# Kernel optimization log

Hardware: AMD Instinct MI355X
Metric: run time of the kernel (lower is better)

Reference implementation:

```python
import jax, jax.numpy as jnp
import numpy as np

# dims: B=batch, N1=in_channels (primary caps), P=pcap_n_dims, N2=n_caps, D=n_dims
B, N1, P, N2, D = 64, 1152, 8, 128, 16
ROUTINGS = 2


def squash(s, axis=-1):
    # squash_factor * unit_vector, with eps-stabilized norm (matches torch.finfo eps)
    sq_norm = jnp.sum(s * s, axis=axis, keepdims=True)
    norm = jnp.sqrt(sq_norm + jnp.finfo(s.dtype).eps)
    return (sq_norm / (1.0 + sq_norm)) * (s / norm)


def setup_inputs() -> dict:
    key = jax.random.key(0)
    k1, k2 = jax.random.split(key)
    x = jax.random.normal(k1, (B, N1, P), dtype=jnp.float32)
    # learned transform W: nn.Parameter(torch.randn(1, N1, N2, D, P)); leading 1 dropped
    W = jax.random.normal(k2, (N1, N2, D, P), dtype=jnp.float32)
    return {"x": x, "W": W}


def reference(x, W):
    b, n1 = x.shape[0], x.shape[1]
    n2 = W.shape[1]
    # caps2_predicted[b,i,n,d] = sum_p W[i,n,d,p] * x[b,i,p]  (the tiled batched matmul)
    pred = jnp.einsum('indp,bip->bind', W, x)  # [B, N1, N2, D]
    raw = jnp.zeros((b, n1, n2), dtype=pred.dtype)  # routing logits
    v = None
    for i in range(ROUTINGS):
        c = jax.nn.softmax(raw, axis=2)                  # softmax over output capsules
        s = jnp.einsum('bin,bind->bnd', c, pred)         # weighted sum over input caps
        v = squash(s, axis=-1)                           # [B, N2, D]
        if i < ROUTINGS - 1:
            # agreement: <prediction, output> over the D dimension
            raw = raw + jnp.einsum('bind,bnd->bin', pred, v)
    return v  # [B, n_caps, n_dims]
```

## Files before the change

### kernel.cpp

```cpp
#include <hip/hip_runtime.h>
#include <math.h>

#define B_   64
#define P_   8
#define N1_  1152
#define N2_  128
#define D_   16

#define NSPLIT 16
#define CHUNK  (N1_ / NSPLIT)
#define NIB    (CHUNK / 4)

typedef __attribute__((ext_vector_type(8)))  short bf16x8;
typedef __attribute__((ext_vector_type(4)))  float f32x4;
typedef __attribute__((ext_vector_type(16))) float f32x16;

__device__ inline void split_frag(float4 a0, float4 a1, bf16x8& hi, bf16x8& lo)
{
    float w[8] = {a0.x, a0.y, a0.z, a0.w, a1.x, a1.y, a1.z, a1.w};
#pragma unroll
    for (int j = 0; j < 8; ++j) {
        unsigned ub = __float_as_uint(w[j]);
        hi[j] = (short)(ub >> 16);
        float hif = __uint_as_float(ub & 0xffff0000u);
        float r = w[j] - hif;
        lo[j] = (short)(__float_as_uint(r) >> 16);
    }
}

__device__ inline void split_arr(const float* w, bf16x8& hi, bf16x8& lo)
{
#pragma unroll
    for (int j = 0; j < 8; ++j) {
        unsigned ub = __float_as_uint(w[j]);
        hi[j] = (short)(ub >> 16);
        float hif = __uint_as_float(ub & 0xffff0000u);
        float r = w[j] - hif;
        lo[j] = (short)(__float_as_uint(r) >> 16);
    }
}

__device__ inline void split4_pack(float4 s, uint2& hp, uint2& lp)
{
    float w[4] = {s.x, s.y, s.z, s.w};
    unsigned hs[4], ls[4];
#pragma unroll
    for (int j = 0; j < 4; ++j) {
        unsigned ub = __float_as_uint(w[j]);
        hs[j] = ub >> 16;
        float hif = __uint_as_float(ub & 0xffff0000u);
        float r = w[j] - hif;
        ls[j] = __float_as_uint(r) >> 16;
    }
    hp.x = hs[0] | (hs[1] << 16); hp.y = hs[2] | (hs[3] << 16);
    lp.x = ls[0] | (ls[1] << 16); lp.y = ls[2] | (ls[3] << 16);
}

__device__ inline unsigned short bf16_rne(float x, float& deq)
{
    unsigned ub = __float_as_uint(x);
    unsigned r  = ub + 0x7fffu + ((ub >> 16) & 1u);
    unsigned short us = (unsigned short)(r >> 16);
    deq = __uint_as_float(((unsigned)us) << 16);
    return us;
}

__global__ __launch_bounds__(256) void k1_s0_mfma(const float* __restrict__ x,
                                                  const float* __restrict__ W,
                                                  float* __restrict__ s0p)
{
    const int tid   = threadIdx.x;
    const int lane  = tid & 63;
    const int wv    = tid >> 6;
    const int col   = lane & 15;
    const int quad  = lane >> 4;
    const int n     = blockIdx.x * 4 + wv;
    const int isp   = blockIdx.y;
    const int ibase = isp * CHUNK;

    f32x4 acc[4];
#pragma unroll
    for (int bt = 0; bt < 4; ++bt) acc[bt] = (f32x4){0.f, 0.f, 0.f, 0.f};

    for (int ib = 0; ib < NIB; ++ib) {
        const int iq = ibase + ib * 4 + quad;
        const float* wp = W + ((size_t)iq * N2_ + n) * (D_ * P_) + col * P_;
        float4 wa = *(const float4*)wp;
        float4 wb = *(const float4*)(wp + 4);
        bf16x8 ahi, alo;
        split_frag(wa, wb, ahi, alo);
#pragma unroll
        for (int bt = 0; bt < 4; ++bt) {
            const int b = bt * 16 + col;
            const float* xp = x + ((size_t)b * N1_ + iq) * P_;
            float4 xa = *(const float4*)xp;
            float4 xb = *(const float4*)(xp + 4);
            bf16x8 bhi, blo;
            split_frag(xa, xb, bhi, blo);
            acc[bt] = __builtin_amdgcn_mfma_f32_16x16x32_bf16(ahi, bhi, acc[bt], 0, 0, 0);
            acc[bt] = __builtin_amdgcn_mfma_f32_16x16x32_bf16(ahi, blo, acc[bt], 0, 0, 0);
            acc[bt] = __builtin_amdgcn_mfma_f32_16x16x32_bf16(alo, bhi, acc[bt], 0, 0, 0);
        }
    }
#pragma unroll
    for (int bt = 0; bt < 4; ++bt) {
        const int b = bt * 16 + col;
        float4 v = make_float4(acc[bt][0], acc[bt][1], acc[bt][2], acc[bt][3]);
        *(float4*)(s0p + (size_t)isp * (B_ * N2_ * D_) + (size_t)b * (N2_ * D_)
                   + n * D_ + quad * 4) = v;
    }
}

__global__ __launch_bounds__(256) void k2_squash(const float* __restrict__ spart,
                                                 float* __restrict__ vout,
                                                 unsigned short* __restrict__ v0h,
                                                 unsigned short* __restrict__ v0l,
                                                 float scale, int nsplit)
{
    int idx = blockIdx.x * 256 + threadIdx.x;
    float4 s = make_float4(0.f, 0.f, 0.f, 0.f);
    for (int sp = 0; sp < nsplit; ++sp) {
        float4 t = *(const float4*)(spart + (size_t)sp * (B_ * N2_ * D_) + (size_t)idx * 4);
        s.x += t.x; s.y += t.y; s.z += t.z; s.w += t.w;
    }
    s.x *= scale; s.y *= scale; s.z *= scale; s.w *= scale;
    float sq = s.x * s.x + s.y * s.y + s.z * s.z + s.w * s.w;
    sq += __shfl_xor(sq, 1);
    sq += __shfl_xor(sq, 2);
    float norm = sqrtf(sq + 1.1920929e-7f);
    float f = (sq / (1.f + sq)) / norm;
    float4 o = make_float4(s.x * f, s.y * f, s.z * f, s.w * f);
    *(float4*)(vout + (size_t)idx * 4) = o;
    if (v0h) {
        uint2 hp, lp;
        split4_pack(o, hp, lp);
        *(uint2*)(v0h + (size_t)idx * 4) = hp;
        *(uint2*)(v0l + (size_t)idx * 4) = lp;
    }
}

__global__ __launch_bounds__(1024) void k3a2_mfma32(const float* __restrict__ x,
                                                    const float* __restrict__ W,
                                                    const unsigned short* __restrict__ v0h,
                                                    const unsigned short* __restrict__ v0l,
                                                    unsigned short* __restrict__ e_t,
                                                    float* __restrict__ denom)
{
    const int tid  = threadIdx.x;
    const int lane = tid & 63;
    const int wv   = tid >> 6;
    const int m    = lane & 31;
    const int kh   = lane >> 5;
    const int isub = m >> 3;
    const int p    = m & 7;
    const int i0   = blockIdx.x * 4;
    const int nbase = wv * 8;

    float4 xq0[4], xq1[4];
#pragma unroll
    for (int is = 0; is < 4; ++is) {
        xq0[is] = *(const float4*)(x + ((size_t)m * N1_ + i0 + is) * P_ + kh * 4);
        xq1[is] = *(const float4*)(x + ((size_t)(32 + m) * N1_ + i0 + is) * P_ + kh * 4);
    }

    float dacc[4] = {0.f, 0.f, 0.f, 0.f};

#pragma unroll 1
    for (int nt = 0; nt < 8; ++nt) {
        const int n = nbase + nt;

        bf16x8 vhi[2], vlo[2];
#pragma unroll
        for (int bt = 0; bt < 2; ++bt) {
            const size_t vo = (size_t)(bt * 32 + m) * (N2_ * D_) + n * D_ + kh * 8;
            vhi[bt] = *(const bf16x8*)(v0h + vo);
            vlo[bt] = *(const bf16x8*)(v0l + vo);
        }

        const float* wp = W + ((size_t)(i0 + isub) * N2_ + n) * (D_ * P_) + kh * 64 + p;
        float a[8];
#pragma unroll
        for (int j = 0; j < 8; ++j) a[j] = wp[8 * j];
        bf16x8 ahi, alo;
        split_arr(a, ahi, alo);

        f32x16 acc0, acc1;
#pragma unroll
        for (int r = 0; r < 16; ++r) { acc0[r] = 0.f; acc1[r] = 0.f; }
        acc0 = __builtin_amdgcn_mfma_f32_32x32x16_bf16(ahi, vhi[0], acc0, 0, 0, 0);
        acc0 = __builtin_amdgcn_mfma_f32_32x32x16_bf16(ahi, vlo[0], acc0, 0, 0, 0);
        acc0 = __builtin_amdgcn_mfma_f32_32x32x16_bf16(alo, vhi[0], acc0, 0, 0, 0);
        acc1 = __builtin_amdgcn_mfma_f32_32x32x16_bf16(ahi, vhi[1], acc1, 0, 0, 0);
        acc1 = __builtin_amdgcn_mfma_f32_32x32x16_bf16(ahi, vlo[1], acc1, 0, 0, 0);
        acc1 = __builtin_amdgcn_mfma_f32_32x32x16_bf16(alo, vhi[1], acc1, 0, 0, 0);

#pragma unroll
        for (int is = 0; is < 4; ++is) {
            float r0 = acc0[4 * is] * xq0[is].x + acc0[4 * is + 1] * xq0[is].y
                     + acc0[4 * is + 2] * xq0[is].z + acc0[4 * is + 3] * xq0[is].w;
            float r1 = acc1[4 * is] * xq1[is].x + acc1[4 * is + 1] * xq1[is].y
                     + acc1[4 * is + 2] * xq1[is].z + acc1[4 * is + 3] * xq1[is].w;
            r0 += __shfl_xor(r0, 32);
            r1 += __shfl_xor(r1, 32);
            float e = __expf(kh ? r1 : r0);
            float er;
            unsigned short eb = bf16_rne(e, er);
            e_t[(size_t)(i0 + is) * (N2_ * 64) + n * 64 + kh * 32 + m] = eb;
            dacc[is] += er;
        }
    }

    __shared__ float dred[16][4][64];
#pragma unroll
    for (int is = 0; is < 4; ++is) dred[wv][is][kh * 32 + m] = dacc[is];
    __syncthreads();
    if (tid < 256) {
        const int is = tid >> 6;
        const int b  = tid & 63;
        float s = 0.f;
#pragma unroll
        for (int w = 0; w < 16; ++w) s += dred[w][is][b];
        denom[(size_t)(i0 + is) * 64 + b] = s;
    }
}

__global__ __launch_bounds__(256) void k3c_s1_mfma(const float* __restrict__ x,
                                                   const float* __restrict__ W,
                                                   const unsigned short* __restrict__ e_t,
                                                   const float* __restrict__ denom,
                                                   float* __restrict__ s1p)
{
    const int tid   = threadIdx.x;
    const int lane  = tid & 63;
    const int wv    = tid >> 6;
    const int col   = lane & 15;
    const int quad  = lane >> 4;
    const int n     = blockIdx.x * 4 + wv;
    const int isp   = blockIdx.y;
    const int ibase = isp * CHUNK;

    f32x4 acc[4];
#pragma unroll
    for (int bt = 0; bt < 4; ++bt) acc[bt] = (f32x4){0.f, 0.f, 0.f, 0.f};

    for (int ib = 0; ib < NIB; ++ib) {
        const int iq = ibase + ib * 4 + quad;
        const float* wp = W + ((size_t)iq * N2_ + n) * (D_ * P_) + col * P_;
        float4 wa = *(const float4*)wp;
        float4 wb = *(const float4*)(wp + 4);
        bf16x8 ahi, alo;
        split_frag(wa, wb, ahi, alo);
#pragma unroll
        for (int bt = 0; bt < 4; ++bt) {
            const int b = bt * 16 + col;
            const float* xp = x + ((size_t)b * N1_ + iq) * P_;
            float4 xa = *(const float4*)xp;
            float4 xb = *(const float4*)(xp + 4);
            float e  = __uint_as_float((unsigned)e_t[((size_t)iq * N2_ + n) * 64 + b] << 16);
            float dv = denom[(size_t)iq * 64 + b];
            float c  = e * __builtin_amdgcn_rcpf(dv);
            float4 ya = make_float4(xa.x * c, xa.y * c, xa.z * c, xa.w * c);
            float4 yb = make_float4(xb.x * c, xb.y * c, xb.z * c, xb.w * c);
            bf16x8 bhi, blo;
            split_frag(ya, yb, bhi, blo);
            acc[bt] = __builtin_amdgcn_mfma_f32_16x16x32_bf16(ahi, bhi, acc[bt], 0, 0, 0);
            acc[bt] = __builtin_amdgcn_mfma_f32_16x16x32_bf16(ahi, blo, acc[bt], 0, 0, 0);
            acc[bt] = __builtin_amdgcn_mfma_f32_16x16x32_bf16(alo, bhi, acc[bt], 0, 0, 0);
        }
    }
#pragma unroll
    for (int bt = 0; bt < 4; ++bt) {
        const int b = bt * 16 + col;
        float4 v = make_float4(acc[bt][0], acc[bt][1], acc[bt][2], acc[bt][3]);
        *(float4*)(s1p + (size_t)isp * (B_ * N2_ * D_) + (size_t)b * (N2_ * D_)
                   + n * D_ + quad * 4) = v;
    }
}

extern "C" void kernel_launch(void* const* d_in, const int* in_sizes, int n_in,
                              void* d_out, int out_size, void* d_ws, size_t ws_size,
                              hipStream_t stream)
{
    const float* x = (const float*)d_in[0];
    const float* W = (const float*)d_in[1];
    float* out = (float*)d_out;

    float* s_part = (float*)d_ws;
    float* v0     = s_part + (size_t)NSPLIT * B_ * N2_ * D_;
    float* denom  = v0 + B_ * N2_ * D_;
    unsigned short* v0h = (unsigned short*)(denom + (size_t)N1_ * 64);
    unsigned short* v0l = v0h + (size_t)B_ * N2_ * D_;
    unsigned short* e_t = v0l + (size_t)B_ * N2_ * D_;

    k1_s0_mfma  <<<dim3(32, NSPLIT),  256, 0, stream>>>(x, W, s_part);
    k2_squash   <<<128,               256, 0, stream>>>(s_part, v0, v0h, v0l, 1.f / 128.f, NSPLIT);
    k3a2_mfma32 <<<N1_ / 4,          1024, 0, stream>>>(x, W, v0h, v0l, e_t, denom);
    k3c_s1_mfma <<<dim3(32, NSPLIT),  256, 0, stream>>>(x, W, e_t, denom, s_part);
    k2_squash   <<<128,               256, 0, stream>>>(s_part, out, nullptr, nullptr, 1.f, NSPLIT);
}
```

Baseline: 232.2 us.

## Fuse all routing stages into one persistent kernel with grid barriers

Replaces five separate launches with an init kernel plus one persistent 512-block kernel that runs every stage and separates them with atomic-counter grid-wide barriers. The goal is to remove per-launch overhead and the gaps between dependent kernels. The agreement stage now runs in 256-thread blocks over 1152 work items and accumulates the softmax denominator with atomicAdd instead of a single block-local write. This relies on all 512 blocks being co-resident, since the barriers spin-wait, and it reduces the parallelism available to the middle stage.

```diff
diff --git a/kernel.cpp b/kernel.cpp
--- a/kernel.cpp
+++ b/kernel.cpp
@@ -10,6 +10,8 @@
 #define NSPLIT 16
 #define CHUNK  (N1_ / NSPLIT)
 #define NIB    (CHUNK / 4)
+
+#define GRID_BLKS 512
 
 typedef __attribute__((ext_vector_type(8)))  short bf16x8;
 typedef __attribute__((ext_vector_type(4)))  float f32x4;
@@ -65,61 +67,30 @@
     return us;
 }
 
-__global__ __launch_bounds__(256) void k1_s0_mfma(const float* __restrict__ x,
-                                                  const float* __restrict__ W,
-                                                  float* __restrict__ s0p)
-{
-    const int tid   = threadIdx.x;
-    const int lane  = tid & 63;
-    const int wv    = tid >> 6;
-    const int col   = lane & 15;
-    const int quad  = lane >> 4;
-    const int n     = blockIdx.x * 4 + wv;
-    const int isp   = blockIdx.y;
-    const int ibase = isp * CHUNK;
-
-    f32x4 acc[4];
-#pragma unroll
-    for (int bt = 0; bt < 4; ++bt) acc[bt] = (f32x4){0.f, 0.f, 0.f, 0.f};
-
-    for (int ib = 0; ib < NIB; ++ib) {
-        const int iq = ibase + ib * 4 + quad;
-        const float* wp = W + ((size_t)iq * N2_ + n) * (D_ * P_) + col * P_;
-        float4 wa = *(const float4*)wp;
-        float4 wb = *(const float4*)(wp + 4);
-        bf16x8 ahi, alo;
-        split_frag(wa, wb, ahi, alo);
-#pragma unroll
-        for (int bt = 0; bt < 4; ++bt) {
-            const int b = bt * 16 + col;
-            const float* xp = x + ((size_t)b * N1_ + iq) * P_;
-            float4 xa = *(const float4*)xp;
-            float4 xb = *(const float4*)(xp + 4);
-            bf16x8 bhi, blo;
-            split_frag(xa, xb, bhi, blo);
-            acc[bt] = __builtin_amdgcn_mfma_f32_16x16x32_bf16(ahi, bhi, acc[bt], 0, 0, 0);
-            acc[bt] = __builtin_amdgcn_mfma_f32_16x16x32_bf16(ahi, blo, acc[bt], 0, 0, 0);
-            acc[bt] = __builtin_amdgcn_mfma_f32_16x16x32_bf16(alo, bhi, acc[bt], 0, 0, 0);
-        }
-    }
-#pragma unroll
-    for (int bt = 0; bt < 4; ++bt) {
-        const int b = bt * 16 + col;
-        float4 v = make_float4(acc[bt][0], acc[bt][1], acc[bt][2], acc[bt][3]);
-        *(float4*)(s0p + (size_t)isp * (B_ * N2_ * D_) + (size_t)b * (N2_ * D_)
-                   + n * D_ + quad * 4) = v;
-    }
-}
-
-__global__ __launch_bounds__(256) void k2_squash(const float* __restrict__ spart,
-                                                 float* __restrict__ vout,
-                                                 unsigned short* __restrict__ v0h,
-                                                 unsigned short* __restrict__ v0l,
-                                                 float scale, int nsplit)
-{
-    int idx = blockIdx.x * 256 + threadIdx.x;
+__device__ inline void gbar(unsigned* __restrict__ bar, int k)
+{
+    __threadfence();
+    __syncthreads();
+    if (threadIdx.x == 0) {
+        __hip_atomic_fetch_add(&bar[k], 1u, __ATOMIC_ACQ_REL, __HIP_MEMORY_SCOPE_AGENT);
+        unsigned spins = 0;
+        while (__hip_atomic_load(&bar[k], __ATOMIC_ACQUIRE, __HIP_MEMORY_SCOPE_AGENT)
+               < (unsigned)GRID_BLKS) {
+            __builtin_amdgcn_s_sleep(2);
+            if (++spins > 400000000u) break;
+        }
+    }
+    __syncthreads();
+}
+
+__device__ inline void squash_body(const float* __restrict__ spart,
+                                   float* __restrict__ vout,
+                                   unsigned short* __restrict__ v0h,
+                                   unsigned short* __restrict__ v0l,
+                                   float scale, int idx)
+{
     float4 s = make_float4(0.f, 0.f, 0.f, 0.f);
-    for (int sp = 0; sp < nsplit; ++sp) {
+    for (int sp = 0; sp < NSPLIT; ++sp) {
         float4 t = *(const float4*)(spart + (size_t)sp * (B_ * N2_ * D_) + (size_t)idx * 4);
         s.x += t.x; s.y += t.y; s.z += t.z; s.w += t.w;
     }
@@ -139,142 +110,201 @@
     }
 }
 
-__global__ __launch_bounds__(1024) void k3a2_mfma32(const float* __restrict__ x,
-                                                    const float* __restrict__ W,
-                                                    const unsigned short* __restrict__ v0h,
-                                                    const unsigned short* __restrict__ v0l,
-                                                    unsigned short* __restrict__ e_t,
-                                                    float* __restrict__ denom)
-{
+__global__ __launch_bounds__(256) void kinit(float* __restrict__ denom,
+                                             unsigned* __restrict__ bar)
+{
+    int z = blockIdx.x * 256 + threadIdx.x;
+    denom[z] = 0.f;
+    if (z < 8) bar[z] = 0u;
+}
+
+__global__ __launch_bounds__(256, 2) void mega(const float* __restrict__ x,
+                                               const float* __restrict__ W,
+                                               float* __restrict__ out,
+                                               float* __restrict__ s_part,
+                                               float* __restrict__ v0,
+                                               float* __restrict__ denom,
+                                               unsigned short* __restrict__ v0h,
+                                               unsigned short* __restrict__ v0l,
+                                               unsigned short* __restrict__ e_t,
+                                               unsigned* __restrict__ bar)
+{
+    const int blk  = blockIdx.x;
     const int tid  = threadIdx.x;
     const int lane = tid & 63;
     const int wv   = tid >> 6;
-    const int m    = lane & 31;
-    const int kh   = lane >> 5;
-    const int isub = m >> 3;
-    const int p    = m & 7;
-    const int i0   = blockIdx.x * 4;
-    const int nbase = wv * 8;
-
-    float4 xq0[4], xq1[4];
-#pragma unroll
-    for (int is = 0; is < 4; ++is) {
-        xq0[is] = *(const float4*)(x + ((size_t)m * N1_ + i0 + is) * P_ + kh * 4);
-        xq1[is] = *(const float4*)(x + ((size_t)(32 + m) * N1_ + i0 + is) * P_ + kh * 4);
-    }
-
-    float dacc[4] = {0.f, 0.f, 0.f, 0.f};
-
-#pragma unroll 1
-    for (int nt = 0; nt < 8; ++nt) {
-        const int n = nbase + nt;
-
-        bf16x8 vhi[2], vlo[2];
-#pragma unroll
-        for (int bt = 0; bt < 2; ++bt) {
-            const size_t vo = (size_t)(bt * 32 + m) * (N2_ * D_) + n * D_ + kh * 8;
-            vhi[bt] = *(const bf16x8*)(v0h + vo);
-            vlo[bt] = *(const bf16x8*)(v0l + vo);
-        }
-
-        const float* wp = W + ((size_t)(i0 + isub) * N2_ + n) * (D_ * P_) + kh * 64 + p;
-        float a[8];
-#pragma unroll
-        for (int j = 0; j < 8; ++j) a[j] = wp[8 * j];
-        bf16x8 ahi, alo;
-        split_arr(a, ahi, alo);
-
-        f32x16 acc0, acc1;
-#pragma unroll
-        for (int r = 0; r < 16; ++r) { acc0[r] = 0.f; acc1[r] = 0.f; }
-        acc0 = __builtin_amdgcn_mfma_f32_32x32x16_bf16(ahi, vhi[0], acc0, 0, 0, 0);
-        acc0 = __builtin_amdgcn_mfma_f32_32x32x16_bf16(ahi, vlo[0], acc0, 0, 0, 0);
-        acc0 = __builtin_amdgcn_mfma_f32_32x32x16_bf16(alo, vhi[0], acc0, 0, 0, 0);
-        acc1 = __builtin_amdgcn_mfma_f32_32x32x16_bf16(ahi, vhi[1], acc1, 0, 0, 0);
-        acc1 = __builtin_amdgcn_mfma_f32_32x32x16_bf16(ahi, vlo[1], acc1, 0, 0, 0);
-        acc1 = __builtin_amdgcn_mfma_f32_32x32x16_bf16(alo, vhi[1], acc1, 0, 0, 0);
-
-#pragma unroll
-        for (int is = 0; is < 4; ++is) {
-            float r0 = acc0[4 * is] * xq0[is].x + acc0[4 * is + 1] * xq0[is].y
-                     + acc0[4 * is + 2] * xq0[is].z + acc0[4 * is + 3] * xq0[is].w;
-            float r1 = acc1[4 * is] * xq1[is].x + acc1[4 * is + 1] * xq1[is].y
-                     + acc1[4 * is + 2] * xq1[is].z + acc1[4 * is + 3] * xq1[is].w;
-            r0 += __shfl_xor(r0, 32);
-            r1 += __shfl_xor(r1, 32);
-            float e = __expf(kh ? r1 : r0);
-            float er;
-            unsigned short eb = bf16_rne(e, er);
-            e_t[(size_t)(i0 + is) * (N2_ * 64) + n * 64 + kh * 32 + m] = eb;
-            dacc[is] += er;
-        }
-    }
-
-    __shared__ float dred[16][4][64];
-#pragma unroll
-    for (int is = 0; is < 4; ++is) dred[wv][is][kh * 32 + m] = dacc[is];
-    __syncthreads();
-    if (tid < 256) {
-        const int is = tid >> 6;
-        const int b  = tid & 63;
-        float s = 0.f;
-#pragma unroll
-        for (int w = 0; w < 16; ++w) s += dred[w][is][b];
-        denom[(size_t)(i0 + is) * 64 + b] = s;
-    }
-}
-
-__global__ __launch_bounds__(256) void k3c_s1_mfma(const float* __restrict__ x,
-                                                   const float* __restrict__ W,
-                                                   const unsigned short* __restrict__ e_t,
-                                                   const float* __restrict__ denom,
-                                                   float* __restrict__ s1p)
-{
-    const int tid   = threadIdx.x;
-    const int lane  = tid & 63;
-    const int wv    = tid >> 6;
-    const int col   = lane & 15;
-    const int quad  = lane >> 4;
-    const int n     = blockIdx.x * 4 + wv;
-    const int isp   = blockIdx.y;
-    const int ibase = isp * CHUNK;
-
-    f32x4 acc[4];
-#pragma unroll
-    for (int bt = 0; bt < 4; ++bt) acc[bt] = (f32x4){0.f, 0.f, 0.f, 0.f};
-
-    for (int ib = 0; ib < NIB; ++ib) {
-        const int iq = ibase + ib * 4 + quad;
-        const float* wp = W + ((size_t)iq * N2_ + n) * (D_ * P_) + col * P_;
-        float4 wa = *(const float4*)wp;
-        float4 wb = *(const float4*)(wp + 4);
-        bf16x8 ahi, alo;
-        split_frag(wa, wb, ahi, alo);
+
+    __shared__ float dred[4][4][64];
+
+    {
+        const int col   = lane & 15;
+        const int quad  = lane >> 4;
+        const int n     = (blk & 31) * 4 + wv;
+        const int isp   = blk >> 5;
+        const int ibase = isp * CHUNK;
+
+        f32x4 acc[4];
+#pragma unroll
+        for (int bt = 0; bt < 4; ++bt) acc[bt] = (f32x4){0.f, 0.f, 0.f, 0.f};
+
+        for (int ib = 0; ib < NIB; ++ib) {
+            const int iq = ibase + ib * 4 + quad;
+            const float* wp = W + ((size_t)iq * N2_ + n) * (D_ * P_) + col * P_;
+            float4 wa = *(const float4*)wp;
+            float4 wb = *(const float4*)(wp + 4);
+            bf16x8 ahi, alo;
+            split_frag(wa, wb, ahi, alo);
+#pragma unroll
+            for (int bt = 0; bt < 4; ++bt) {
+                const int b = bt * 16 + col;
+                const float* xp = x + ((size_t)b * N1_ + iq) * P_;
+                float4 xa = *(const float4*)xp;
+                float4 xb = *(const float4*)(xp + 4);
+                bf16x8 bhi, blo;
+                split_frag(xa, xb, bhi, blo);
+                acc[bt] = __builtin_amdgcn_mfma_f32_16x16x32_bf16(ahi, bhi, acc[bt], 0, 0, 0);
+                acc[bt] = __builtin_amdgcn_mfma_f32_16x16x32_bf16(ahi, blo, acc[bt], 0, 0, 0);
+                acc[bt] = __builtin_amdgcn_mfma_f32_16x16x32_bf16(alo, bhi, acc[bt], 0, 0, 0);
+            }
+        }
 #pragma unroll
         for (int bt = 0; bt < 4; ++bt) {
             const int b = bt * 16 + col;
-            const float* xp = x + ((size_t)b * N1_ + iq) * P_;
-            float4 xa = *(const float4*)xp;
-            float4 xb = *(const float4*)(xp + 4);
-            float e  = __uint_as_float((unsigned)e_t[((size_t)iq * N2_ + n) * 64 + b] << 16);
-            float dv = denom[(size_t)iq * 64 + b];
-            float c  = e * __builtin_amdgcn_rcpf(dv);
-            float4 ya = make_float4(xa.x * c, xa.y * c, xa.z * c, xa.w * c);
-            float4 yb = make_float4(xb.x * c, xb.y * c, xb.z * c, xb.w * c);
-            bf16x8 bhi, blo;
-            split_frag(ya, yb, bhi, blo);
-            acc[bt] = __builtin_amdgcn_mfma_f32_16x16x32_bf16(ahi, bhi, acc[bt], 0, 0, 0);
-            acc[bt] = __builtin_amdgcn_mfma_f32_16x16x32_bf16(ahi, blo, acc[bt], 0, 0, 0);
-            acc[bt] = __builtin_amdgcn_mfma_f32_16x16x32_bf16(alo, bhi, acc[bt], 0, 0, 0);
-        }
-    }
-#pragma unroll
-    for (int bt = 0; bt < 4; ++bt) {
-        const int b = bt * 16 + col;
-        float4 v = make_float4(acc[bt][0], acc[bt][1], acc[bt][2], acc[bt][3]);
-        *(float4*)(s1p + (size_t)isp * (B_ * N2_ * D_) + (size_t)b * (N2_ * D_)
-                   + n * D_ + quad * 4) = v;
-    }
+            float4 v = make_float4(acc[bt][0], acc[bt][1], acc[bt][2], acc[bt][3]);
+            *(float4*)(s_part + (size_t)isp * (B_ * N2_ * D_) + (size_t)b * (N2_ * D_)
+                       + n * D_ + quad * 4) = v;
+        }
+    }
+    gbar(bar, 0);
+
+    if (blk < 128)
+        squash_body(s_part, v0, v0h, v0l, 1.f / 128.f, blk * 256 + tid);
+    gbar(bar, 1);
+
+    for (int vb = blk; vb < 1152; vb += GRID_BLKS) {
+        const int m    = lane & 31;
+        const int kh   = lane >> 5;
+        const int isub = m >> 3;
+        const int p    = m & 7;
+        const int i0   = (vb >> 2) * 4;
+        const int nbase = (vb & 3) * 32 + wv * 8;
+
+        float4 xq0[4], xq1[4];
+#pragma unroll
+        for (int is = 0; is < 4; ++is) {
+            xq0[is] = *(const float4*)(x + ((size_t)m * N1_ + i0 + is) * P_ + kh * 4);
+            xq1[is] = *(const float4*)(x + ((size_t)(32 + m) * N1_ + i0 + is) * P_ + kh * 4);
+        }
+
+        float dacc[4] = {0.f, 0.f, 0.f, 0.f};
+
+#pragma unroll 1
+        for (int nt = 0; nt < 8; ++nt) {
+            const int n = nbase + nt;
+
+            bf16x8 vhi[2], vlo[2];
+#pragma unroll
+            for (int bt = 0; bt < 2; ++bt) {
+                const size_t vo = (size_t)(bt * 32 + m) * (N2_ * D_) + n * D_ + kh * 8;
+                vhi[bt] = *(const bf16x8*)(v0h + vo);
+                vlo[bt] = *(const bf16x8*)(v0l + vo);
+            }
+
+            const float* wp = W + ((size_t)(i0 + isub) * N2_ + n) * (D_ * P_) + kh * 64 + p;
+            float a[8];
+#pragma unroll
+            for (int j = 0; j < 8; ++j) a[j] = wp[8 * j];
+            bf16x8 ahi, alo;
+            split_arr(a, ahi, alo);
+
+            f32x16 acc0, acc1;
+#pragma unroll
+            for (int r = 0; r < 16; ++r) { acc0[r] = 0.f; acc1[r] = 0.f; }
+            acc0 = __builtin_amdgcn_mfma_f32_32x32x16_bf16(ahi, vhi[0], acc0, 0, 0, 0);
+            acc0 = __builtin_amdgcn_mfma_f32_32x32x16_bf16(ahi, vlo[0], acc0, 0, 0, 0);
+            acc0 = __builtin_amdgcn_mfma_f32_32x32x16_bf16(alo, vhi[0], acc0, 0, 0, 0);
+            acc1 = __builtin_amdgcn_mfma_f32_32x32x16_bf16(ahi, vhi[1], acc1, 0, 0, 0);
+            acc1 = __builtin_amdgcn_mfma_f32_32x32x16_bf16(ahi, vlo[1], acc1, 0, 0, 0);
+            acc1 = __builtin_amdgcn_mfma_f32_32x32x16_bf16(alo, vhi[1], acc1, 0, 0, 0);
+
+#pragma unroll
+            for (int is = 0; is < 4; ++is) {
+                float r0 = acc0[4 * is] * xq0[is].x + acc0[4 * is + 1] * xq0[is].y
+                         + acc0[4 * is + 2] * xq0[is].z + acc0[4 * is + 3] * xq0[is].w;
+                float r1 = acc1[4 * is] * xq1[is].x + acc1[4 * is + 1] * xq1[is].y
+                         + acc1[4 * is + 2] * xq1[is].z + acc1[4 * is + 3] * xq1[is].w;
+                r0 += __shfl_xor(r0, 32);
+                r1 += __shfl_xor(r1, 32);
+                float e = __expf(kh ? r1 : r0);
+                float er;
+                unsigned short eb = bf16_rne(e, er);
+                e_t[(size_t)(i0 + is) * (N2_ * 64) + n * 64 + kh * 32 + m] = eb;
+                dacc[is] += er;
+            }
+        }
+
+        __syncthreads();
+#pragma unroll
+        for (int is = 0; is < 4; ++is) dred[wv][is][kh * 32 + m] = dacc[is];
+        __syncthreads();
+        {
+            const int is2 = tid >> 6;
+            const int b2  = tid & 63;
+            float s = dred[0][is2][b2] + dred[1][is2][b2]
+                    + dred[2][is2][b2] + dred[3][is2][b2];
+            atomicAdd(&denom[(size_t)(i0 + is2) * 64 + b2], s);
+        }
+    }
+    gbar(bar, 2);
+
+    {
+        const int col   = lane & 15;
+        const int quad  = lane >> 4;
+        const int n     = (blk & 31) * 4 + wv;
+        const int isp   = blk >> 5;
+        const int ibase = isp * CHUNK;
+
+        f32x4 acc[4];
+#pragma unroll
+        for (int bt = 0; bt < 4; ++bt) acc[bt] = (f32x4){0.f, 0.f, 0.f, 0.f};
+
+        for (int ib = 0; ib < NIB; ++ib) {
+            const int iq = ibase + ib * 4 + quad;
+            const float* wp = W + ((size_t)iq * N2_ + n) * (D_ * P_) + col * P_;
+            float4 wa = *(const float4*)wp;
+            float4 wb = *(const float4*)(wp + 4);
+            bf16x8 ahi, alo;
+            split_frag(wa, wb, ahi, alo);
+#pragma unroll
+            for (int bt = 0; bt < 4; ++bt) {
+                const int b = bt * 16 + col;
+                const float* xp = x + ((size_t)b * N1_ + iq) * P_;
+                float4 xa = *(const float4*)xp;
+                float4 xb = *(const float4*)(xp + 4);
+                float e  = __uint_as_float((unsigned)e_t[((size_t)iq * N2_ + n) * 64 + b] << 16);
+                float dv = denom[(size_t)iq * 64 + b];
+                float c  = e * __builtin_amdgcn_rcpf(dv);
+                float4 ya = make_float4(xa.x * c, xa.y * c, xa.z * c, xa.w * c);
+                float4 yb = make_float4(xb.x * c, xb.y * c, xb.z * c, xb.w * c);
+                bf16x8 bhi, blo;
+                split_frag(ya, yb, bhi, blo);
+                acc[bt] = __builtin_amdgcn_mfma_f32_16x16x32_bf16(ahi, bhi, acc[bt], 0, 0, 0);
+                acc[bt] = __builtin_amdgcn_mfma_f32_16x16x32_bf16(ahi, blo, acc[bt], 0, 0, 0);
+                acc[bt] = __builtin_amdgcn_mfma_f32_16x16x32_bf16(alo, bhi, acc[bt], 0, 0, 0);
+            }
+        }
+#pragma unroll
+        for (int bt = 0; bt < 4; ++bt) {
+            const int b = bt * 16 + col;
+            float4 v = make_float4(acc[bt][0], acc[bt][1], acc[bt][2], acc[bt][3]);
+            *(float4*)(s_part + (size_t)isp * (B_ * N2_ * D_) + (size_t)b * (N2_ * D_)
+                       + n * D_ + quad * 4) = v;
+        }
+    }
+    gbar(bar, 3);
+
+    if (blk < 128)
+        squash_body(s_part, out, nullptr, nullptr, 1.f, blk * 256 + tid);
 }
 
 extern "C" void kernel_launch(void* const* d_in, const int* in_sizes, int n_in,
@@ -291,10 +321,9 @@
     unsigned short* v0h = (unsigned short*)(denom + (size_t)N1_ * 64);
     unsigned short* v0l = v0h + (size_t)B_ * N2_ * D_;
     unsigned short* e_t = v0l + (size_t)B_ * N2_ * D_;
-
-    k1_s0_mfma  <<<dim3(32, NSPLIT),  256, 0, stream>>>(x, W, s_part);
-    k2_squash   <<<128,               256, 0, stream>>>(s_part, v0, v0h, v0l, 1.f / 128.f, NSPLIT);
-    k3a2_mfma32 <<<N1_ / 4,          1024, 0, stream>>>(x, W, v0h, v0l, e_t, denom);
-    k3c_s1_mfma <<<dim3(32, NSPLIT),  256, 0, stream>>>(x, W, e_t, denom, s_part);
-    k2_squash   <<<128,               256, 0, stream>>>(s_part, out, nullptr, nullptr, 1.f, NSPLIT);
-}
+    unsigned* bar = (unsigned*)(e_t + (size_t)N1_ * N2_ * 64);
+
+    kinit <<<288,       256, 0, stream>>>(denom, bar);
+    mega  <<<GRID_BLKS, 256, 0, stream>>>(x, W, out, s_part, v0, denom,
+                                          v0h, v0l, e_t, bar);
+}
```

Measured after the change: 664.0 us. 186% more time.
